# Kernel tuning notes

Measured on AMD Instinct MI355X. Metric: run time of the kernel, lower is better.

The kernel has to match this reference:

```python
import jax, jax.numpy as jnp
import numpy as np

N = 10000    # nodes
D = 128      # d_model
K = 16       # d_state
S = 5        # seq_len (tokens per node)
E = 320000   # edges
R = 200      # num relation types
P = E // (S - 1)  # edges sampled per tokenizer step
EPS = 1e-5


def setup_inputs() -> dict:
    key = jax.random.key(0)
    ks = jax.random.split(key, 16)
    sc = 1.0 / np.sqrt(D)
    return {
        "x": jax.random.normal(ks[0], (N, D), jnp.float32),
        "edge_index": jax.random.randint(ks[1], (2, E), 0, N),
        "edge_type": jax.random.randint(ks[2], (E,), 0, R),
        "perms": jax.random.randint(ks[3], (S - 1, P), 0, E),
        "rel_table": jax.random.normal(ks[4], (R, D), jnp.float32) * 0.1,
        "log_A": jax.random.normal(ks[5], (D, K), jnp.float32) * 0.1,
        "W_B": jax.random.normal(ks[6], (D, K), jnp.float32) * sc,
        "W_C": jax.random.normal(ks[7], (D, K), jnp.float32) * sc,
        "W_delta": jax.random.normal(ks[8], (D, D), jnp.float32) * sc,
        "b_delta": jnp.zeros((D,), jnp.float32),
        "W_g": jax.random.normal(ks[9], (D, D), jnp.float32) * sc,
        "b_g": jnp.zeros((D,), jnp.float32),
        "W_out": jax.random.normal(ks[10], (D, D), jnp.float32) * sc,
        "b_out": jnp.zeros((D,), jnp.float32),
        "ln_g": jnp.ones((D,), jnp.float32),
        "ln_b": jnp.zeros((D,), jnp.float32),
    }


def _tokenize(x, edge_index, edge_type, perms, rel_table):
    # x: [N,D]; perms: [S-1,P] -> tokens [N,S,D]
    src, dst = edge_index[0], edge_index[1]
    step_src = src[perms]                    # [S-1,P]
    step_dst = dst[perms]                    # [S-1,P]
    msg = x[step_src] + rel_table[edge_type[perms]]  # [S-1,P,D]
    seg = jax.vmap(lambda i, m: jax.ops.segment_sum(m, i, num_segments=N))(step_dst, msg)  # [S-1,N,D]
    deg = jax.vmap(lambda i: jax.ops.segment_sum(jnp.ones((P,), x.dtype), i, num_segments=N))(step_dst)  # [S-1,N]
    neigh = seg / jnp.clip(deg, 1.0)[..., None]
    return jnp.concatenate([x[:, None, :], jnp.moveaxis(neigh, 0, 1)], axis=1)  # [N,S,D]


def _selective_scan(tokens, log_A, W_B, W_C, W_delta, b_delta):
    # tokens: [N,S,D] -> [N,S,D]
    deltas = jax.nn.softplus(tokens @ W_delta + b_delta)  # [N,S,D]
    Bs = tokens @ W_B                                     # [N,S,K]
    Cs = tokens @ W_C                                     # [N,S,K]
    A_cont = -jnp.exp(log_A)                              # [D,K]
    A_disc = jnp.exp(deltas[..., None] * A_cont)          # [N,S,D,K]
    Bx = deltas[..., None] * Bs[:, :, None, :] * tokens[..., None]  # [N,S,D,K] = B_disc * x_k

    def step(state, xs):
        a, bx, c = xs                          # [N,D,K],[N,D,K],[N,K]
        state = a * state + bx
        y = jnp.einsum('ndk,nk->nd', state, c)
        return state, y

    init = jnp.zeros((tokens.shape[0], D, K), tokens.dtype)
    _, ys = jax.lax.scan(step, init, (jnp.moveaxis(A_disc, 1, 0),
                                      jnp.moveaxis(Bx, 1, 0),
                                      jnp.moveaxis(Cs, 1, 0)))
    return jnp.moveaxis(ys, 0, 1)  # [N,S,D]


def reference(x, edge_index, edge_type, perms, rel_table, log_A, W_B, W_C,
              W_delta, b_delta, W_g, b_g, W_out, b_out, ln_g, ln_b):
    tokens = _tokenize(x, edge_index, edge_type, perms, rel_table)
    out_f = _selective_scan(tokens, log_A, W_B, W_C, W_delta, b_delta)
    out_b = _selective_scan(tokens[:, ::-1, :], log_A, W_B, W_C, W_delta, b_delta)
    scan_out = (out_f + out_b[:, ::-1, :]).mean(axis=1)  # [N,D]
    gate = jax.nn.silu(x @ W_g + b_g)
    res = x + gate * (scan_out @ W_out + b_out)
    mu = res.mean(axis=-1, keepdims=True)
    var = res.var(axis=-1, keepdims=True)
    return (res - mu) / jnp.sqrt(var + EPS) * ln_g + ln_b
```

## Files before the change

### kernel.cpp

```cpp
#include <hip/hip_runtime.h>
#include <hip/hip_bf16.h>
#include <math.h>

#define N_NODES 10000
#define D_MODEL 128
#define E_EDGES 320000
#define P_EDGES 80000
#define LN_EPS 1e-5f
#define NBUCK 40960
#define CAP 32
#define M_ROWS 50000
#define M_PAD  50048
#define NPAD   320

typedef __attribute__((ext_vector_type(8))) short bf16x8;
typedef __attribute__((ext_vector_type(4))) float f32x4;

__device__ __forceinline__ unsigned short f2bf(float f) {
    __hip_bfloat16 h = __float2bfloat16(f);
    return *reinterpret_cast<unsigned short*>(&h);
}
__device__ __forceinline__ float bf2f(unsigned int u) {
    return __uint_as_float(u << 16);
}

__global__ __launch_bounds__(256) void prep_all(
    const float* __restrict__ Wd, const float* __restrict__ Wb,
    const float* __restrict__ Wc, const float* __restrict__ Wg,
    const float* __restrict__ W_out,
    const float* __restrict__ x, const float* __restrict__ rel,
    const int* __restrict__ edge_index, const int* __restrict__ edge_type,
    unsigned short* __restrict__ Bp, unsigned short* __restrict__ Wop,
    unsigned short* __restrict__ x_bf, unsigned short* __restrict__ rel_bf,
    int* __restrict__ cnt, int4* __restrict__ ed4)
{
    int gid = blockIdx.x * 256 + threadIdx.x;
    if (gid < 40960) {
        int k = gid / NPAD, n = gid - (gid / NPAD) * NPAD;
        float v = 0.f;
        if (n < 128)      v = Wd[k * 128 + n];
        else if (n < 144) v = Wb[k * 16 + (n - 128)];
        else if (n < 160) v = Wc[k * 16 + (n - 144)];
        else if (n < 288) v = Wg[k * 128 + (n - 160)];
        Bp[((size_t)(k >> 3) * NPAD + n) * 8 + (k & 7)] = f2bf(v);
    } else if (gid < 57344) {
        int i = gid - 40960;
        int k = i >> 7, n = i & 127;
        Wop[((size_t)(k >> 3) * 128 + n) * 8 + (k & 7)] = f2bf(W_out[k * 128 + n]);
    } else if (gid < 98304) {
        cnt[gid - 57344] = 0;
    } else if (gid < 123904) {
        int i = gid - 98304;
        rel_bf[i] = f2bf(rel[i]);
    } else if (gid < 1403904) {
        int i = gid - 123904;
        x_bf[i] = f2bf(x[i]);
    } else if (gid < 1723904) {
        int e = gid - 1403904;
        ed4[e] = make_int4(edge_index[e], edge_index[E_EDGES + e], edge_type[e], 0);
    }
}

__global__ __launch_bounds__(256) void csr_build(
    const int4* __restrict__ ed4, const int* __restrict__ perms,
    int* __restrict__ cnt, int2* __restrict__ slots)
{
    int gid = blockIdx.x * blockDim.x + threadIdx.x;
    if (gid >= 4 * P_EDGES) return;
    int s = gid / P_EDGES;
    int e = perms[gid];
    int4 ed = ed4[e];
    int b = ed.y * 4 + s;
    int pos = atomicAdd(&cnt[b], 1);
    if (pos < CAP) slots[(size_t)b * CAP + pos] = make_int2(ed.x, ed.z);
}

__global__ __launch_bounds__(256) void gather_tokens(
    const unsigned short* __restrict__ x_bf,
    const int* __restrict__ cnt, const int2* __restrict__ slots,
    const unsigned short* __restrict__ rel_bf,
    unsigned short* __restrict__ tokens)
{
    int n = blockIdx.x;
    int w = threadIdx.x >> 6, lane = threadIdx.x & 63;
    int b = n * 4 + w;
    int c = cnt[b];
    int cc = c < CAP ? c : CAP;
    const int2* sl = slots + (size_t)b * CAP;
    const unsigned int* xu = (const unsigned int*)x_bf;
    const unsigned int* ru = (const unsigned int*)rel_bf;
    float ax = 0.f, ay = 0.f;
    int j = 0;
    for (; j + 4 <= cc; j += 4) {
        int4 e01 = *(const int4*)(sl + j);
        int4 e23 = *(const int4*)(sl + j + 2);
        unsigned int x0 = xu[(size_t)e01.x * 64 + lane];
        unsigned int r0 = ru[(size_t)e01.y * 64 + lane];
        unsigned int x1 = xu[(size_t)e01.z * 64 + lane];
        unsigned int r1 = ru[(size_t)e01.w * 64 + lane];
        unsigned int x2 = xu[(size_t)e23.x * 64 + lane];
        unsigned int r2 = ru[(size_t)e23.y * 64 + lane];
        unsigned int x3 = xu[(size_t)e23.z * 64 + lane];
        unsigned int r3 = ru[(size_t)e23.w * 64 + lane];
        ax += (bf2f(x0 & 0xffffu) + bf2f(r0 & 0xffffu))
            + (bf2f(x1 & 0xffffu) + bf2f(r1 & 0xffffu))
            + (bf2f(x2 & 0xffffu) + bf2f(r2 & 0xffffu))
            + (bf2f(x3 & 0xffffu) + bf2f(r3 & 0xffffu));
        ay += (bf2f(x0 >> 16) + bf2f(r0 >> 16))
            + (bf2f(x1 >> 16) + bf2f(r1 >> 16))
            + (bf2f(x2 >> 16) + bf2f(r2 >> 16))
            + (bf2f(x3 >> 16) + bf2f(r3 >> 16));
    }
    if (j + 2 <= cc) {
        int4 e01 = *(const int4*)(sl + j);
        unsigned int x0 = xu[(size_t)e01.x * 64 + lane];
        unsigned int r0 = ru[(size_t)e01.y * 64 + lane];
        unsigned int x1 = xu[(size_t)e01.z * 64 + lane];
        unsigned int r1 = ru[(size_t)e01.w * 64 + lane];
        ax += (bf2f(x0 & 0xffffu) + bf2f(r0 & 0xffffu))
            + (bf2f(x1 & 0xffffu) + bf2f(r1 & 0xffffu));
        ay += (bf2f(x0 >> 16) + bf2f(r0 >> 16))
            + (bf2f(x1 >> 16) + bf2f(r1 >> 16));
        j += 2;
    }
    if (j < cc) {
        int2 se = sl[j];
        unsigned int xa = xu[(size_t)se.x * 64 + lane];
        unsigned int ra = ru[(size_t)se.y * 64 + lane];
        ax += bf2f(xa & 0xffffu) + bf2f(ra & 0xffffu);
        ay += bf2f(xa >> 16) + bf2f(ra >> 16);
    }
    float inv = 1.f / fmaxf((float)c, 1.f);
    unsigned int pack = (unsigned int)f2bf(ax * inv)
                      | ((unsigned int)f2bf(ay * inv) << 16);
    ((unsigned int*)tokens)[((size_t)n * 5 + w + 1) * 64 + lane] = pack;
    if (w == 0)
        ((unsigned int*)tokens)[((size_t)n * 5) * 64 + lane] = xu[(size_t)n * 64 + lane];
}

__global__ __launch_bounds__(256) void mfma_gemm(
    const unsigned short* __restrict__ tokens,
    const unsigned short* __restrict__ Bp,
    const float* __restrict__ b_delta, const float* __restrict__ b_g,
    unsigned short* __restrict__ delta,
    unsigned short* __restrict__ bc,
    unsigned short* __restrict__ g)
{
    int m0 = blockIdx.x * 64, n0 = blockIdx.y * 64;
    int wv = threadIdx.x >> 6, lane = threadIdx.x & 63;
    int quad = lane >> 4, l16 = lane & 15;

    f32x4 acc[4] = {{0,0,0,0},{0,0,0,0},{0,0,0,0},{0,0,0,0}};
    const unsigned short* arow = tokens + (size_t)(m0 + wv * 16 + l16) * 128 + quad * 8;
    #pragma unroll
    for (int kc = 0; kc < 128; kc += 32) {
        bf16x8 a = *(const bf16x8*)(arow + kc);
        #pragma unroll
        for (int t = 0; t < 4; ++t) {
            bf16x8 b = *(const bf16x8*)(Bp + ((size_t)(kc / 8 + quad) * NPAD + n0 + 16 * t + l16) * 8);
            acc[t] = __builtin_amdgcn_mfma_f32_16x16x32_bf16(a, b, acc[t], 0, 0, 0);
        }
    }

    int rbase = m0 + wv * 16 + quad * 4;
    #pragma unroll
    for (int t = 0; t < 4; ++t) {
        int c = n0 + 16 * t + l16;
        #pragma unroll
        for (int reg = 0; reg < 4; ++reg) {
            int r = rbase + reg;
            if (r >= M_ROWS) continue;
            float v = acc[t][reg];
            if (c < 128) {
                float z = v + b_delta[c];
                float d = (z > 15.f) ? z : log1pf(__expf(z));
                delta[(size_t)r * 128 + c] = f2bf(d);
            } else if (c < 160) {
                bc[(size_t)r * 32 + (c - 128)] = f2bf(v);
            } else if (c < 288) {
                int rq = r / 5;
                if (r - rq * 5 == 0)
                    g[(size_t)rq * 128 + (c - 160)] = f2bf(v + b_g[c - 160]);
            }
        }
    }
}

__global__ __launch_bounds__(256) void scan_out(
    const unsigned short* __restrict__ tokens,
    const unsigned short* __restrict__ delta,
    const unsigned short* __restrict__ bcbuf,
    const float* __restrict__ log_A,
    const unsigned short* __restrict__ Wop,
    const unsigned short* __restrict__ gbuf,
    const float* __restrict__ x,
    const float* __restrict__ b_out,
    const float* __restrict__ ln_g, const float* __restrict__ ln_b,
    float* __restrict__ out)
{
    int m0 = blockIdx.x * 16;
    int t = threadIdx.x;

    __shared__ float BCs[16][160];
    __shared__ unsigned short soL[16][128];
    __shared__ float res[16 * 132];
    __shared__ float pmu[16][16];
    __shared__ float pv2[16][16];
    __shared__ float muA[16], rstdA[16];

    for (int idx = t; idx < 2560; idx += 256) {
        int n = idx / 160, rem = idx - n * 160;
        int s = rem >> 5, q = rem & 31;
        BCs[n][rem] = bf2f(bcbuf[((size_t)(m0 + n) * 5 + s) * 32 + q]);
    }

    const int d = t & 127;
    float Ac[16];
    {
        const float4* la = (const float4*)(log_A + d * 16);
        #pragma unroll
        for (int q = 0; q < 4; ++q) {
            float4 lv = la[q];
            Ac[q * 4 + 0] = -__expf(lv.x);
            Ac[q * 4 + 1] = -__expf(lv.y);
            Ac[q * 4 + 2] = -__expf(lv.z);
            Ac[q * 4 + 3] = -__expf(lv.w);
        }
    }
    __syncthreads();

    #pragma unroll 1
    for (int i = 0; i < 8; ++i) {
        int n = 2 * i + (t >> 7);
        const unsigned short* tb = tokens + ((size_t)(m0 + n) * 5) * 128 + d;
        const unsigned short* db = delta  + ((size_t)(m0 + n) * 5) * 128 + d;
        float tv[5], dl[5];
        #pragma unroll
        for (int s = 0; s < 5; ++s) {
            tv[s] = bf2f(tb[s * 128]);
            dl[s] = bf2f(db[s * 128]);
        }
        const float* BCn = BCs[n];

        float Af[5][16];
        float total = 0.f;
        {
            float st[16];
            #pragma unroll
            for (int k = 0; k < 16; ++k) st[k] = 0.f;
            #pragma unroll
            for (int s = 0; s < 5; ++s) {
                float dtv = dl[s] * tv[s];
                float y = 0.f;
                #pragma unroll
                for (int k = 0; k < 16; ++k) {
                    float A = __expf(dl[s] * Ac[k]);
                    Af[s][k] = A;
                    st[k] = fmaf(A, st[k], dtv * BCn[s * 32 + k]);
                    y = fmaf(st[k], BCn[s * 32 + 16 + k], y);
                }
                total += y;
            }
        }
        {
            float st[16];
            #pragma unroll
            for (int k = 0; k < 16; ++k) st[k] = 0.f;
            #pragma unroll
            for (int s = 4; s >= 0; --s) {
                float dtv = dl[s] * tv[s];
                float y = 0.f;
                #pragma unroll
                for (int k = 0; k < 16; ++k) {
                    st[k] = fmaf(Af[s][k], st[k], dtv * BCn[s * 32 + k]);
                    y = fmaf(st[k], BCn[s * 32 + 16 + k], y);
                }
                total += y;
            }
        }
        soL[n][d] = f2bf(total * 0.2f);
    }
    __syncthreads();

    int wv = t >> 6, lane = t & 63;
    int quad = lane >> 4, l16 = lane & 15;
    f32x4 acc[2] = {{0,0,0,0},{0,0,0,0}};
    #pragma unroll
    for (int kc = 0; kc < 128; kc += 32) {
        bf16x8 a = *(const bf16x8*)&soL[l16][kc + quad * 8];
        #pragma unroll
        for (int tt = 0; tt < 2; ++tt) {
            int tc = wv * 2 + tt;
            bf16x8 b = *(const bf16x8*)(Wop + ((size_t)(kc / 8 + quad) * 128 + 16 * tc + l16) * 8);
            acc[tt] = __builtin_amdgcn_mfma_f32_16x16x32_bf16(a, b, acc[tt], 0, 0, 0);
        }
    }

    #pragma unroll
    for (int tt = 0; tt < 2; ++tt) {
        int c = wv * 32 + tt * 16 + l16;
        #pragma unroll
        for (int reg = 0; reg < 4; ++reg) {
            int lrow = quad * 4 + reg;
            int r = m0 + lrow;
            float o = acc[tt][reg] + b_out[c];
            float gl = bf2f(gbuf[(size_t)r * 128 + c]);
            float gate = gl / (1.f + __expf(-gl));
            res[lrow * 132 + c] = x[(size_t)r * 128 + c] + gate * o;
        }
    }
    __syncthreads();

    {
        int row = t >> 4, q = t & 15;
        float s = 0.f, s2 = 0.f;
        #pragma unroll
        for (int i = 0; i < 8; ++i) {
            float v = res[row * 132 + q + 16 * i];
            s += v; s2 += v * v;
        }
        pmu[row][q] = s; pv2[row][q] = s2;
    }
    __syncthreads();
    if (t < 16) {
        float s = 0.f, s2 = 0.f;
        #pragma unroll
        for (int i = 0; i < 16; ++i) { s += pmu[t][i]; s2 += pv2[t][i]; }
        float mu = s * (1.f / 128.f);
        float var = s2 * (1.f / 128.f) - mu * mu;
        muA[t] = mu;
        rstdA[t] = rsqrtf(var + LN_EPS);
    }
    __syncthreads();
    #pragma unroll
    for (int i = 0; i < 8; ++i) {
        int idx = i * 256 + t;
        int row = idx >> 7, c = idx & 127;
        out[(size_t)(m0 + row) * 128 + c] =
            (res[row * 132 + c] - muA[row]) * rstdA[row] * ln_g[c] + ln_b[c];
    }
}

extern "C" void kernel_launch(void* const* d_in, const int* in_sizes, int n_in,
                              void* d_out, int out_size, void* d_ws, size_t ws_size,
                              hipStream_t stream) {
    const float* x          = (const float*)d_in[0];
    const int*   edge_index = (const int*)  d_in[1];
    const int*   edge_type  = (const int*)  d_in[2];
    const int*   perms      = (const int*)  d_in[3];
    const float* rel_table  = (const float*)d_in[4];
    const float* log_A      = (const float*)d_in[5];
    const float* W_B        = (const float*)d_in[6];
    const float* W_C        = (const float*)d_in[7];
    const float* W_delta    = (const float*)d_in[8];
    const float* b_delta    = (const float*)d_in[9];
    const float* W_g        = (const float*)d_in[10];
    const float* b_g        = (const float*)d_in[11];
    const float* W_out      = (const float*)d_in[12];
    const float* b_out      = (const float*)d_in[13];
    const float* ln_g       = (const float*)d_in[14];
    const float* ln_b       = (const float*)d_in[15];

    char* ws = (char*)d_ws;
    int*            cnt    = (int*)           (ws + 0);
    unsigned short* Bp     = (unsigned short*)(ws + 163840);
    unsigned short* Wop    = (unsigned short*)(ws + 245760);
    unsigned short* x_bf   = (unsigned short*)(ws + 278528);
    unsigned short* rel_bf = (unsigned short*)(ws + 2838528);
    int4*           ed4    = (int4*)          (ws + 2889728);
    unsigned short* tokens = (unsigned short*)(ws + 8009728);
    unsigned short* g      = (unsigned short*)(ws + 20822016);
    unsigned short* bc     = (unsigned short*)(ws + 23382016);
    int2*           slots  = (int2*)          (ws + 26582016);
    unsigned short* delta  = (unsigned short*)(ws + 26582016);

    prep_all<<<(1723904 + 255) / 256, 256, 0, stream>>>(
        W_delta, W_B, W_C, W_g, W_out, x, rel_table, edge_index, edge_type,
        Bp, Wop, x_bf, rel_bf, cnt, ed4);

    csr_build<<<(4 * P_EDGES + 255) / 256, 256, 0, stream>>>(
        ed4, perms, cnt, slots);

    gather_tokens<<<N_NODES, 256, 0, stream>>>(
        x_bf, cnt, slots, rel_bf, tokens);

    mfma_gemm<<<dim3(M_PAD / 64, NPAD / 64), 256, 0, stream>>>(
        tokens, Bp, b_delta, b_g, delta, bc, g);

    scan_out<<<N_NODES / 16, 256, 0, stream>>>(
        tokens, delta, bc, log_A, Wop, g, x, b_out, ln_g, ln_b, (float*)d_out);
}
```

Baseline: 202.4 us.

## Fuse token gather, projection GEMM and scan into one per-tile kernel

Merges the gather_tokens, mfma_gemm and scan_out kernels into a single kernel that handles 16 nodes per block. Tokens, deltas, B/C and gate values stay in shared memory instead of going through global workspace buffers, which removes two launches and the global round trips of the intermediates. In exchange each block uses about 66KB of LDS, which limits occupancy, and the gather phase now runs on only 625 blocks, so less parallelism is available to hide latency on the irregular loads.

```diff
diff --git a/kernel.cpp b/kernel.cpp
--- a/kernel.cpp
+++ b/kernel.cpp
@@ -9,9 +9,7 @@
 #define LN_EPS 1e-5f
 #define NBUCK 40960
 #define CAP 32
-#define M_ROWS 50000
-#define M_PAD  50048
-#define NPAD   320
+#define NPAD 320
 
 typedef __attribute__((ext_vector_type(8))) short bf16x8;
 typedef __attribute__((ext_vector_type(4))) float f32x4;
@@ -75,144 +73,127 @@
     if (pos < CAP) slots[(size_t)b * CAP + pos] = make_int2(ed.x, ed.z);
 }
 
-__global__ __launch_bounds__(256) void gather_tokens(
+#define TOKS 136
+__global__ __launch_bounds__(256, 2) void fused_main(
     const unsigned short* __restrict__ x_bf,
     const int* __restrict__ cnt, const int2* __restrict__ slots,
     const unsigned short* __restrict__ rel_bf,
-    unsigned short* __restrict__ tokens)
-{
-    int n = blockIdx.x;
-    int w = threadIdx.x >> 6, lane = threadIdx.x & 63;
-    int b = n * 4 + w;
-    int c = cnt[b];
-    int cc = c < CAP ? c : CAP;
-    const int2* sl = slots + (size_t)b * CAP;
-    const unsigned int* xu = (const unsigned int*)x_bf;
-    const unsigned int* ru = (const unsigned int*)rel_bf;
-    float ax = 0.f, ay = 0.f;
-    int j = 0;
-    for (; j + 4 <= cc; j += 4) {
-        int4 e01 = *(const int4*)(sl + j);
-        int4 e23 = *(const int4*)(sl + j + 2);
-        unsigned int x0 = xu[(size_t)e01.x * 64 + lane];
-        unsigned int r0 = ru[(size_t)e01.y * 64 + lane];
-        unsigned int x1 = xu[(size_t)e01.z * 64 + lane];
-        unsigned int r1 = ru[(size_t)e01.w * 64 + lane];
-        unsigned int x2 = xu[(size_t)e23.x * 64 + lane];
-        unsigned int r2 = ru[(size_t)e23.y * 64 + lane];
-        unsigned int x3 = xu[(size_t)e23.z * 64 + lane];
-        unsigned int r3 = ru[(size_t)e23.w * 64 + lane];
-        ax += (bf2f(x0 & 0xffffu) + bf2f(r0 & 0xffffu))
-            + (bf2f(x1 & 0xffffu) + bf2f(r1 & 0xffffu))
-            + (bf2f(x2 & 0xffffu) + bf2f(r2 & 0xffffu))
-            + (bf2f(x3 & 0xffffu) + bf2f(r3 & 0xffffu));
-        ay += (bf2f(x0 >> 16) + bf2f(r0 >> 16))
-            + (bf2f(x1 >> 16) + bf2f(r1 >> 16))
-            + (bf2f(x2 >> 16) + bf2f(r2 >> 16))
-            + (bf2f(x3 >> 16) + bf2f(r3 >> 16));
-    }
-    if (j + 2 <= cc) {
-        int4 e01 = *(const int4*)(sl + j);
-        unsigned int x0 = xu[(size_t)e01.x * 64 + lane];
-        unsigned int r0 = ru[(size_t)e01.y * 64 + lane];
-        unsigned int x1 = xu[(size_t)e01.z * 64 + lane];
-        unsigned int r1 = ru[(size_t)e01.w * 64 + lane];
-        ax += (bf2f(x0 & 0xffffu) + bf2f(r0 & 0xffffu))
-            + (bf2f(x1 & 0xffffu) + bf2f(r1 & 0xffffu));
-        ay += (bf2f(x0 >> 16) + bf2f(r0 >> 16))
-            + (bf2f(x1 >> 16) + bf2f(r1 >> 16));
-        j += 2;
-    }
-    if (j < cc) {
-        int2 se = sl[j];
-        unsigned int xa = xu[(size_t)se.x * 64 + lane];
-        unsigned int ra = ru[(size_t)se.y * 64 + lane];
-        ax += bf2f(xa & 0xffffu) + bf2f(ra & 0xffffu);
-        ay += bf2f(xa >> 16) + bf2f(ra >> 16);
-    }
-    float inv = 1.f / fmaxf((float)c, 1.f);
-    unsigned int pack = (unsigned int)f2bf(ax * inv)
-                      | ((unsigned int)f2bf(ay * inv) << 16);
-    ((unsigned int*)tokens)[((size_t)n * 5 + w + 1) * 64 + lane] = pack;
-    if (w == 0)
-        ((unsigned int*)tokens)[((size_t)n * 5) * 64 + lane] = xu[(size_t)n * 64 + lane];
-}
-
-__global__ __launch_bounds__(256) void mfma_gemm(
-    const unsigned short* __restrict__ tokens,
     const unsigned short* __restrict__ Bp,
+    const unsigned short* __restrict__ Wop,
+    const float* __restrict__ log_A,
     const float* __restrict__ b_delta, const float* __restrict__ b_g,
-    unsigned short* __restrict__ delta,
-    unsigned short* __restrict__ bc,
-    unsigned short* __restrict__ g)
-{
-    int m0 = blockIdx.x * 64, n0 = blockIdx.y * 64;
-    int wv = threadIdx.x >> 6, lane = threadIdx.x & 63;
-    int quad = lane >> 4, l16 = lane & 15;
-
-    f32x4 acc[4] = {{0,0,0,0},{0,0,0,0},{0,0,0,0},{0,0,0,0}};
-    const unsigned short* arow = tokens + (size_t)(m0 + wv * 16 + l16) * 128 + quad * 8;
-    #pragma unroll
-    for (int kc = 0; kc < 128; kc += 32) {
-        bf16x8 a = *(const bf16x8*)(arow + kc);
-        #pragma unroll
-        for (int t = 0; t < 4; ++t) {
-            bf16x8 b = *(const bf16x8*)(Bp + ((size_t)(kc / 8 + quad) * NPAD + n0 + 16 * t + l16) * 8);
-            acc[t] = __builtin_amdgcn_mfma_f32_16x16x32_bf16(a, b, acc[t], 0, 0, 0);
-        }
-    }
-
-    int rbase = m0 + wv * 16 + quad * 4;
-    #pragma unroll
-    for (int t = 0; t < 4; ++t) {
-        int c = n0 + 16 * t + l16;
-        #pragma unroll
-        for (int reg = 0; reg < 4; ++reg) {
-            int r = rbase + reg;
-            if (r >= M_ROWS) continue;
-            float v = acc[t][reg];
-            if (c < 128) {
-                float z = v + b_delta[c];
-                float d = (z > 15.f) ? z : log1pf(__expf(z));
-                delta[(size_t)r * 128 + c] = f2bf(d);
-            } else if (c < 160) {
-                bc[(size_t)r * 32 + (c - 128)] = f2bf(v);
-            } else if (c < 288) {
-                int rq = r / 5;
-                if (r - rq * 5 == 0)
-                    g[(size_t)rq * 128 + (c - 160)] = f2bf(v + b_g[c - 160]);
-            }
-        }
-    }
-}
-
-__global__ __launch_bounds__(256) void scan_out(
-    const unsigned short* __restrict__ tokens,
-    const unsigned short* __restrict__ delta,
-    const unsigned short* __restrict__ bcbuf,
-    const float* __restrict__ log_A,
-    const unsigned short* __restrict__ Wop,
-    const unsigned short* __restrict__ gbuf,
     const float* __restrict__ x,
     const float* __restrict__ b_out,
     const float* __restrict__ ln_g, const float* __restrict__ ln_b,
     float* __restrict__ out)
 {
-    int m0 = blockIdx.x * 16;
-    int t = threadIdx.x;
-
-    __shared__ float BCs[16][160];
-    __shared__ unsigned short soL[16][128];
-    __shared__ float res[16 * 132];
-    __shared__ float pmu[16][16];
-    __shared__ float pv2[16][16];
-    __shared__ float muA[16], rstdA[16];
-
-    for (int idx = t; idx < 2560; idx += 256) {
-        int n = idx / 160, rem = idx - n * 160;
-        int s = rem >> 5, q = rem & 31;
-        BCs[n][rem] = bf2f(bcbuf[((size_t)(m0 + n) * 5 + s) * 32 + q]);
-    }
+    const int n0 = blockIdx.x * 16;
+    const int t = threadIdx.x;
+    const int wv = t >> 6, lane = t & 63;
+    const int quad = lane >> 4, l16 = lane & 15;
+
+    __shared__ __align__(16) char smem[66304];
+    unsigned short* tokL = (unsigned short*)smem;
+    unsigned short* dltL = (unsigned short*)(smem + 21760);
+    float*          bcL  = (float*)(smem + 43520);
+    float*          gL   = (float*)(smem + 53760);
+    unsigned short* soL  = (unsigned short*)(smem + 61952);
+    float* res   = (float*)smem;
+    float* pmu   = (float*)(smem + 8448);
+    float* pv2   = (float*)(smem + 9472);
+    float* muA   = (float*)(smem + 10496);
+    float* rstdA = (float*)(smem + 10560);
+
+    const unsigned int* xu = (const unsigned int*)x_bf;
+    const unsigned int* ru = (const unsigned int*)rel_bf;
+
+    for (int idx = t; idx < 1024; idx += 256) {
+        int i = idx >> 6, ln2 = idx & 63;
+        ((unsigned int*)&tokL[(i * 5) * TOKS])[ln2] = xu[(size_t)(n0 + i) * 64 + ln2];
+    }
+    for (int q = 0; q < 16; ++q) {
+        int bl = wv * 16 + q;
+        int i = bl >> 2, s = bl & 3;
+        int B = (n0 + i) * 4 + s;
+        int c = cnt[B];
+        int cc = c < CAP ? c : CAP;
+        const int2* sl = slots + (size_t)B * CAP;
+        float ax = 0.f, ay = 0.f;
+        int j = 0;
+        for (; j + 4 <= cc; j += 4) {
+            int4 e01 = *(const int4*)(sl + j);
+            int4 e23 = *(const int4*)(sl + j + 2);
+            unsigned int x0 = xu[(size_t)e01.x * 64 + lane];
+            unsigned int r0 = ru[(size_t)e01.y * 64 + lane];
+            unsigned int x1 = xu[(size_t)e01.z * 64 + lane];
+            unsigned int r1 = ru[(size_t)e01.w * 64 + lane];
+            unsigned int x2 = xu[(size_t)e23.x * 64 + lane];
+            unsigned int r2 = ru[(size_t)e23.y * 64 + lane];
+            unsigned int x3 = xu[(size_t)e23.z * 64 + lane];
+            unsigned int r3 = ru[(size_t)e23.w * 64 + lane];
+            ax += (bf2f(x0 & 0xffffu) + bf2f(r0 & 0xffffu))
+                + (bf2f(x1 & 0xffffu) + bf2f(r1 & 0xffffu))
+                + (bf2f(x2 & 0xffffu) + bf2f(r2 & 0xffffu))
+                + (bf2f(x3 & 0xffffu) + bf2f(r3 & 0xffffu));
+            ay += (bf2f(x0 >> 16) + bf2f(r0 >> 16))
+                + (bf2f(x1 >> 16) + bf2f(r1 >> 16))
+                + (bf2f(x2 >> 16) + bf2f(r2 >> 16))
+                + (bf2f(x3 >> 16) + bf2f(r3 >> 16));
+        }
+        if (j + 2 <= cc) {
+            int4 e01 = *(const int4*)(sl + j);
+            unsigned int x0 = xu[(size_t)e01.x * 64 + lane];
+            unsigned int r0 = ru[(size_t)e01.y * 64 + lane];
+            unsigned int x1 = xu[(size_t)e01.z * 64 + lane];
+            unsigned int r1 = ru[(size_t)e01.w * 64 + lane];
+            ax += (bf2f(x0 & 0xffffu) + bf2f(r0 & 0xffffu))
+                + (bf2f(x1 & 0xffffu) + bf2f(r1 & 0xffffu));
+            ay += (bf2f(x0 >> 16) + bf2f(r0 >> 16))
+                + (bf2f(x1 >> 16) + bf2f(r1 >> 16));
+            j += 2;
+        }
+        if (j < cc) {
+            int2 se = sl[j];
+            unsigned int xa = xu[(size_t)se.x * 64 + lane];
+            unsigned int ra = ru[(size_t)se.y * 64 + lane];
+            ax += bf2f(xa & 0xffffu) + bf2f(ra & 0xffffu);
+            ay += bf2f(xa >> 16) + bf2f(ra >> 16);
+        }
+        float inv = 1.f / fmaxf((float)c, 1.f);
+        unsigned int pack = (unsigned int)f2bf(ax * inv)
+                          | ((unsigned int)f2bf(ay * inv) << 16);
+        *(unsigned int*)&tokL[(i * 5 + s + 1) * TOKS + 2 * lane] = pack;
+    }
+    __syncthreads();
+
+    for (int tt = wv; tt < 90; tt += 4) {
+        int mt = tt / 18, nt = tt - mt * 18;
+        f32x4 acc = {0, 0, 0, 0};
+        #pragma unroll
+        for (int kc = 0; kc < 4; ++kc) {
+            bf16x8 a = *(const bf16x8*)&tokL[(mt * 16 + l16) * TOKS + kc * 32 + quad * 8];
+            bf16x8 b = *(const bf16x8*)(Bp + ((size_t)(kc * 4 + quad) * NPAD + nt * 16 + l16) * 8);
+            acc = __builtin_amdgcn_mfma_f32_16x16x32_bf16(a, b, acc, 0, 0, 0);
+        }
+        int c = nt * 16 + l16;
+        #pragma unroll
+        for (int reg = 0; reg < 4; ++reg) {
+            int lr = mt * 16 + quad * 4 + reg;
+            float v = acc[reg];
+            if (c < 128) {
+                float z = v + b_delta[c];
+                float d = (z > 15.f) ? z : log1pf(__expf(z));
+                dltL[lr * TOKS + c] = f2bf(d);
+            } else if (c < 160) {
+                bcL[lr * 32 + (c - 128)] = v;
+            } else {
+                int rq = lr / 5;
+                if (lr - rq * 5 == 0)
+                    gL[rq * 128 + (c - 160)] = v + b_g[c - 160];
+            }
+        }
+    }
+    __syncthreads();
 
     const int d = t & 127;
     float Ac[16];
@@ -227,20 +208,16 @@
             Ac[q * 4 + 3] = -__expf(lv.w);
         }
     }
-    __syncthreads();
-
     #pragma unroll 1
     for (int i = 0; i < 8; ++i) {
-        int n = 2 * i + (t >> 7);
-        const unsigned short* tb = tokens + ((size_t)(m0 + n) * 5) * 128 + d;
-        const unsigned short* db = delta  + ((size_t)(m0 + n) * 5) * 128 + d;
+        int nl = 2 * i + (t >> 7);
         float tv[5], dl[5];
         #pragma unroll
         for (int s = 0; s < 5; ++s) {
-            tv[s] = bf2f(tb[s * 128]);
-            dl[s] = bf2f(db[s * 128]);
-        }
-        const float* BCn = BCs[n];
+            tv[s] = bf2f(tokL[(nl * 5 + s) * TOKS + d]);
+            dl[s] = bf2f(dltL[(nl * 5 + s) * TOKS + d]);
+        }
+        const float* BCn = &bcL[nl * 5 * 32];
 
         float Af[5][16];
         float total = 0.f;
@@ -278,35 +255,42 @@
                 total += y;
             }
         }
-        soL[n][d] = f2bf(total * 0.2f);
-    }
-    __syncthreads();
-
-    int wv = t >> 6, lane = t & 63;
-    int quad = lane >> 4, l16 = lane & 15;
+        soL[nl * TOKS + d] = f2bf(total * 0.2f);
+    }
+    __syncthreads();
+
     f32x4 acc[2] = {{0,0,0,0},{0,0,0,0}};
     #pragma unroll
-    for (int kc = 0; kc < 128; kc += 32) {
-        bf16x8 a = *(const bf16x8*)&soL[l16][kc + quad * 8];
+    for (int kc = 0; kc < 4; ++kc) {
+        bf16x8 a = *(const bf16x8*)&soL[l16 * TOKS + kc * 32 + quad * 8];
         #pragma unroll
         for (int tt = 0; tt < 2; ++tt) {
             int tc = wv * 2 + tt;
-            bf16x8 b = *(const bf16x8*)(Wop + ((size_t)(kc / 8 + quad) * 128 + 16 * tc + l16) * 8);
+            bf16x8 b = *(const bf16x8*)(Wop + ((size_t)(kc * 4 + quad) * 128 + 16 * tc + l16) * 8);
             acc[tt] = __builtin_amdgcn_mfma_f32_16x16x32_bf16(a, b, acc[tt], 0, 0, 0);
         }
     }
-
+    float rv[2][4];
     #pragma unroll
     for (int tt = 0; tt < 2; ++tt) {
         int c = wv * 32 + tt * 16 + l16;
         #pragma unroll
         for (int reg = 0; reg < 4; ++reg) {
             int lrow = quad * 4 + reg;
-            int r = m0 + lrow;
             float o = acc[tt][reg] + b_out[c];
-            float gl = bf2f(gbuf[(size_t)r * 128 + c]);
+            float gl = gL[lrow * 128 + c];
             float gate = gl / (1.f + __expf(-gl));
-            res[lrow * 132 + c] = x[(size_t)r * 128 + c] + gate * o;
+            rv[tt][reg] = x[(size_t)(n0 + lrow) * 128 + c] + gate * o;
+        }
+    }
+    __syncthreads();
+    #pragma unroll
+    for (int tt = 0; tt < 2; ++tt) {
+        int c = wv * 32 + tt * 16 + l16;
+        #pragma unroll
+        for (int reg = 0; reg < 4; ++reg) {
+            int lrow = quad * 4 + reg;
+            res[lrow * 132 + c] = rv[tt][reg];
         }
     }
     __syncthreads();
@@ -319,13 +303,13 @@
             float v = res[row * 132 + q + 16 * i];
             s += v; s2 += v * v;
         }
-        pmu[row][q] = s; pv2[row][q] = s2;
+        pmu[row * 16 + q] = s; pv2[row * 16 + q] = s2;
     }
     __syncthreads();
     if (t < 16) {
         float s = 0.f, s2 = 0.f;
         #pragma unroll
-        for (int i = 0; i < 16; ++i) { s += pmu[t][i]; s2 += pv2[t][i]; }
+        for (int i = 0; i < 16; ++i) { s += pmu[t * 16 + i]; s2 += pv2[t * 16 + i]; }
         float mu = s * (1.f / 128.f);
         float var = s2 * (1.f / 128.f) - mu * mu;
         muA[t] = mu;
@@ -336,7 +320,7 @@
     for (int i = 0; i < 8; ++i) {
         int idx = i * 256 + t;
         int row = idx >> 7, c = idx & 127;
-        out[(size_t)(m0 + row) * 128 + c] =
+        out[(size_t)(n0 + row) * 128 + c] =
             (res[row * 132 + c] - muA[row]) * rstdA[row] * ln_g[c] + ln_b[c];
     }
 }
@@ -368,11 +352,7 @@
     unsigned short* x_bf   = (unsigned short*)(ws + 278528);
     unsigned short* rel_bf = (unsigned short*)(ws + 2838528);
     int4*           ed4    = (int4*)          (ws + 2889728);
-    unsigned short* tokens = (unsigned short*)(ws + 8009728);
-    unsigned short* g      = (unsigned short*)(ws + 20822016);
-    unsigned short* bc     = (unsigned short*)(ws + 23382016);
-    int2*           slots  = (int2*)          (ws + 26582016);
-    unsigned short* delta  = (unsigned short*)(ws + 26582016);
+    int2*           slots  = (int2*)          (ws + 8009728);
 
     prep_all<<<(1723904 + 255) / 256, 256, 0, stream>>>(
         W_delta, W_B, W_C, W_g, W_out, x, rel_table, edge_index, edge_type,
@@ -381,12 +361,7 @@
     csr_build<<<(4 * P_EDGES + 255) / 256, 256, 0, stream>>>(
         ed4, perms, cnt, slots);
 
-    gather_tokens<<<N_NODES, 256, 0, stream>>>(
-        x_bf, cnt, slots, rel_bf, tokens);
-
-    mfma_gemm<<<dim3(M_PAD / 64, NPAD / 64), 256, 0, stream>>>(
-        tokens, Bp, b_delta, b_g, delta, bc, g);
-
-    scan_out<<<N_NODES / 16, 256, 0, stream>>>(
-        tokens, delta, bc, log_A, Wop, g, x, b_out, ln_g, ln_b, (float*)d_out);
-}
+    fused_main<<<N_NODES / 16, 256, 0, stream>>>(
+        x_bf, cnt, slots, rel_bf, Bp, Wop, log_A, b_delta, b_g,
+        x, b_out, ln_g, ln_b, (float*)d_out);
+}
```

New measurement: 256.7 us. 1.27x slower.

## Widen scan_out to 512 threads, alias shared memory, write x token in prep

Applied to the files above, without the earlier changes.

scan_out now runs with 512 threads per block. Each thread processes 4 node-rows instead of 8, and each wave computes a single 16-column MFMA tile for the output projection. Shared memory is packed into one aliased buffer, with the residual tile overlapping the BC staging area. A padded soL stride reduces LDS bank conflicts. The copy of x into token slot 0 moves from gather_tokens into prep_all. The changes aim to raise parallelism and occupancy in the scan epilogue and remove redundant work from gather, but they add a redundant zero store and rely on an extra barrier to make the aliasing safe.

```diff
diff --git a/kernel.cpp b/kernel.cpp
--- a/kernel.cpp
+++ b/kernel.cpp
@@ -32,7 +32,8 @@
     const int* __restrict__ edge_index, const int* __restrict__ edge_type,
     unsigned short* __restrict__ Bp, unsigned short* __restrict__ Wop,
     unsigned short* __restrict__ x_bf, unsigned short* __restrict__ rel_bf,
-    int* __restrict__ cnt, int4* __restrict__ ed4)
+    int* __restrict__ cnt, int4* __restrict__ ed4,
+    unsigned short* __restrict__ tokens)
 {
     int gid = blockIdx.x * 256 + threadIdx.x;
     if (gid < 40960) {
@@ -54,7 +55,9 @@
         rel_bf[i] = f2bf(rel[i]);
     } else if (gid < 1403904) {
         int i = gid - 123904;
-        x_bf[i] = f2bf(x[i]);
+        unsigned short v = f2bf(x[i]);
+        x_bf[i] = v;
+        tokens[(size_t)(i >> 7) * 640 + (i & 127)] = v;
     } else if (gid < 1723904) {
         int e = gid - 1403904;
         ed4[e] = make_int4(edge_index[e], edge_index[E_EDGES + e], edge_type[e], 0);
@@ -134,8 +137,6 @@
     unsigned int pack = (unsigned int)f2bf(ax * inv)
                       | ((unsigned int)f2bf(ay * inv) << 16);
     ((unsigned int*)tokens)[((size_t)n * 5 + w + 1) * 64 + lane] = pack;
-    if (w == 0)
-        ((unsigned int*)tokens)[((size_t)n * 5) * 64 + lane] = xu[(size_t)n * 64 + lane];
 }
 
 __global__ __launch_bounds__(256) void mfma_gemm(
@@ -186,7 +187,8 @@
     }
 }
 
-__global__ __launch_bounds__(256) void scan_out(
+#define SOS 136
+__global__ __launch_bounds__(512) void scan_out(
     const unsigned short* __restrict__ tokens,
     const unsigned short* __restrict__ delta,
     const unsigned short* __restrict__ bcbuf,
@@ -198,20 +200,25 @@
     const float* __restrict__ ln_g, const float* __restrict__ ln_b,
     float* __restrict__ out)
 {
-    int m0 = blockIdx.x * 16;
-    int t = threadIdx.x;
-
-    __shared__ float BCs[16][160];
-    __shared__ unsigned short soL[16][128];
-    __shared__ float res[16 * 132];
-    __shared__ float pmu[16][16];
-    __shared__ float pv2[16][16];
-    __shared__ float muA[16], rstdA[16];
-
-    for (int idx = t; idx < 2560; idx += 256) {
+    const int m0 = blockIdx.x * 16;
+    const int t = threadIdx.x;
+    const int wv = t >> 6, lane = t & 63;
+    const int quad = lane >> 4, l16 = lane & 15;
+
+    __shared__ __align__(16) char smem[19136];
+    float*          BCs = (float*)smem;
+    unsigned short* soL = (unsigned short*)(smem + 10240);
+    float* pmu   = (float*)(smem + 14592);
+    float* pv2   = (float*)(smem + 16640);
+    float* muA   = (float*)(smem + 18688);
+    float* rstdA = (float*)(smem + 18752);
+    float* res   = (float*)smem;
+
+    for (int idx = t; idx < 2560; idx += 512) {
         int n = idx / 160, rem = idx - n * 160;
         int s = rem >> 5, q = rem & 31;
-        BCs[n][rem] = bf2f(bcbuf[((size_t)(m0 + n) * 5 + s) * 32 + q]);
+        BCs[n * 160 + rem - (s << 5) + s * 32 + q - q] = 0.f;
+        BCs[n * 160 + rem] = bf2f(bcbuf[((size_t)(m0 + n) * 5 + s) * 32 + q]);
     }
 
     const int d = t & 127;
@@ -230,17 +237,17 @@
     __syncthreads();
 
     #pragma unroll 1
-    for (int i = 0; i < 8; ++i) {
-        int n = 2 * i + (t >> 7);
-        const unsigned short* tb = tokens + ((size_t)(m0 + n) * 5) * 128 + d;
-        const unsigned short* db = delta  + ((size_t)(m0 + n) * 5) * 128 + d;
+    for (int i = 0; i < 4; ++i) {
+        int nl = 4 * i + (t >> 7);
+        const unsigned short* tb = tokens + ((size_t)(m0 + nl) * 5) * 128 + d;
+        const unsigned short* db = delta  + ((size_t)(m0 + nl) * 5) * 128 + d;
         float tv[5], dl[5];
         #pragma unroll
         for (int s = 0; s < 5; ++s) {
             tv[s] = bf2f(tb[s * 128]);
             dl[s] = bf2f(db[s * 128]);
         }
-        const float* BCn = BCs[n];
+        const float* BCn = &BCs[nl * 160];
 
         float Af[5][16];
         float total = 0.f;
@@ -278,54 +285,52 @@
                 total += y;
             }
         }
-        soL[n][d] = f2bf(total * 0.2f);
-    }
-    __syncthreads();
-
-    int wv = t >> 6, lane = t & 63;
-    int quad = lane >> 4, l16 = lane & 15;
-    f32x4 acc[2] = {{0,0,0,0},{0,0,0,0}};
+        soL[nl * SOS + d] = f2bf(total * 0.2f);
+    }
+    __syncthreads();
+
+    f32x4 acc = {0, 0, 0, 0};
     #pragma unroll
-    for (int kc = 0; kc < 128; kc += 32) {
-        bf16x8 a = *(const bf16x8*)&soL[l16][kc + quad * 8];
-        #pragma unroll
-        for (int tt = 0; tt < 2; ++tt) {
-            int tc = wv * 2 + tt;
-            bf16x8 b = *(const bf16x8*)(Wop + ((size_t)(kc / 8 + quad) * 128 + 16 * tc + l16) * 8);
-            acc[tt] = __builtin_amdgcn_mfma_f32_16x16x32_bf16(a, b, acc[tt], 0, 0, 0);
-        }
-    }
-
-    #pragma unroll
-    for (int tt = 0; tt < 2; ++tt) {
-        int c = wv * 32 + tt * 16 + l16;
+    for (int kc = 0; kc < 4; ++kc) {
+        bf16x8 a = *(const bf16x8*)&soL[l16 * SOS + kc * 32 + quad * 8];
+        bf16x8 b = *(const bf16x8*)(Wop + ((size_t)(kc * 4 + quad) * 128 + 16 * wv + l16) * 8);
+        acc = __builtin_amdgcn_mfma_f32_16x16x32_bf16(a, b, acc, 0, 0, 0);
+    }
+    {
+        int c = wv * 16 + l16;
+        float rv[4];
         #pragma unroll
         for (int reg = 0; reg < 4; ++reg) {
             int lrow = quad * 4 + reg;
-            int r = m0 + lrow;
-            float o = acc[tt][reg] + b_out[c];
-            float gl = bf2f(gbuf[(size_t)r * 128 + c]);
+            float o = acc[reg] + b_out[c];
+            float gl = bf2f(gbuf[(size_t)(m0 + lrow) * 128 + c]);
             float gate = gl / (1.f + __expf(-gl));
-            res[lrow * 132 + c] = x[(size_t)r * 128 + c] + gate * o;
+            rv[reg] = x[(size_t)(m0 + lrow) * 128 + c] + gate * o;
+        }
+        __syncthreads();
+        #pragma unroll
+        for (int reg = 0; reg < 4; ++reg) {
+            int lrow = quad * 4 + reg;
+            res[lrow * 132 + c] = rv[reg];
         }
     }
     __syncthreads();
 
     {
-        int row = t >> 4, q = t & 15;
+        int row = t >> 5, q = t & 31;
         float s = 0.f, s2 = 0.f;
         #pragma unroll
-        for (int i = 0; i < 8; ++i) {
-            float v = res[row * 132 + q + 16 * i];
+        for (int i = 0; i < 4; ++i) {
+            float v = res[row * 132 + q + 32 * i];
             s += v; s2 += v * v;
         }
-        pmu[row][q] = s; pv2[row][q] = s2;
+        pmu[row * 32 + q] = s; pv2[row * 32 + q] = s2;
     }
     __syncthreads();
     if (t < 16) {
         float s = 0.f, s2 = 0.f;
         #pragma unroll
-        for (int i = 0; i < 16; ++i) { s += pmu[t][i]; s2 += pv2[t][i]; }
+        for (int i = 0; i < 32; ++i) { s += pmu[t * 32 + i]; s2 += pv2[t * 32 + i]; }
         float mu = s * (1.f / 128.f);
         float var = s2 * (1.f / 128.f) - mu * mu;
         muA[t] = mu;
@@ -333,8 +338,8 @@
     }
     __syncthreads();
     #pragma unroll
-    for (int i = 0; i < 8; ++i) {
-        int idx = i * 256 + t;
+    for (int i = 0; i < 4; ++i) {
+        int idx = i * 512 + t;
         int row = idx >> 7, c = idx & 127;
         out[(size_t)(m0 + row) * 128 + c] =
             (res[row * 132 + c] - muA[row]) * rstdA[row] * ln_g[c] + ln_b[c];
@@ -376,7 +381,7 @@
 
     prep_all<<<(1723904 + 255) / 256, 256, 0, stream>>>(
         W_delta, W_B, W_C, W_g, W_out, x, rel_table, edge_index, edge_type,
-        Bp, Wop, x_bf, rel_bf, cnt, ed4);
+        Bp, Wop, x_bf, rel_bf, cnt, ed4, tokens);
 
     csr_build<<<(4 * P_EDGES + 255) / 256, 256, 0, stream>>>(
         ed4, perms, cnt, slots);
@@ -387,6 +392,6 @@
     mfma_gemm<<<dim3(M_PAD / 64, NPAD / 64), 256, 0, stream>>>(
         tokens, Bp, b_delta, b_g, delta, bc, g);
 
-    scan_out<<<N_NODES / 16, 256, 0, stream>>>(
+    scan_out<<<N_NODES / 16, 512, 0, stream>>>(
         tokens, delta, bc, log_A, Wop, g, x, b_out, ln_g, ln_b, (float*)d_out);
 }
```

Result: slower. 211.1 us (+4.3%).

## Fuse forward and backward scans into one pass, write token 0 in prep

Applied to the files above, without the earlier changes.

The backward selective scan is folded into the forward loop algebraically. A running suffix vector V of C values, decayed by the same A factors, gives the backward contribution as dtv*dot(V,B). This drops the stored Af[5][16] array and the second pass of 80 FMAs per node-channel, which cuts register pressure. Separately, prep_all now writes the bf16 copy of x directly into token slot 0, so gather_tokens no longer does that extra read and write. The rewritten reduction changes floating-point summation order slightly.

```diff
diff --git a/kernel.cpp b/kernel.cpp
--- a/kernel.cpp
+++ b/kernel.cpp
@@ -32,7 +32,8 @@
     const int* __restrict__ edge_index, const int* __restrict__ edge_type,
     unsigned short* __restrict__ Bp, unsigned short* __restrict__ Wop,
     unsigned short* __restrict__ x_bf, unsigned short* __restrict__ rel_bf,
-    int* __restrict__ cnt, int4* __restrict__ ed4)
+    int* __restrict__ cnt, int4* __restrict__ ed4,
+    unsigned short* __restrict__ tokens)
 {
     int gid = blockIdx.x * 256 + threadIdx.x;
     if (gid < 40960) {
@@ -54,7 +55,9 @@
         rel_bf[i] = f2bf(rel[i]);
     } else if (gid < 1403904) {
         int i = gid - 123904;
-        x_bf[i] = f2bf(x[i]);
+        unsigned short v = f2bf(x[i]);
+        x_bf[i] = v;
+        tokens[(size_t)(i >> 7) * 640 + (i & 127)] = v;
     } else if (gid < 1723904) {
         int e = gid - 1403904;
         ed4[e] = make_int4(edge_index[e], edge_index[E_EDGES + e], edge_type[e], 0);
@@ -134,8 +137,6 @@
     unsigned int pack = (unsigned int)f2bf(ax * inv)
                       | ((unsigned int)f2bf(ay * inv) << 16);
     ((unsigned int*)tokens)[((size_t)n * 5 + w + 1) * 64 + lane] = pack;
-    if (w == 0)
-        ((unsigned int*)tokens)[((size_t)n * 5) * 64 + lane] = xu[(size_t)n * 64 + lane];
 }
 
 __global__ __launch_bounds__(256) void mfma_gemm(
@@ -186,6 +187,7 @@
     }
 }
 
+#define SOS 136
 __global__ __launch_bounds__(256) void scan_out(
     const unsigned short* __restrict__ tokens,
     const unsigned short* __restrict__ delta,
@@ -198,14 +200,15 @@
     const float* __restrict__ ln_g, const float* __restrict__ ln_b,
     float* __restrict__ out)
 {
-    int m0 = blockIdx.x * 16;
-    int t = threadIdx.x;
-
-    __shared__ float BCs[16][160];
-    __shared__ unsigned short soL[16][128];
-    __shared__ float res[16 * 132];
-    __shared__ float pmu[16][16];
-    __shared__ float pv2[16][16];
+    const int m0 = blockIdx.x * 16;
+    const int t = threadIdx.x;
+    const int wv = t >> 6, lane = t & 63;
+    const int quad = lane >> 4, l16 = lane & 15;
+
+    __shared__ __align__(16) float BCs[16][160];
+    __shared__ __align__(16) unsigned short soL[16][SOS];
+    __shared__ float res[16][132];
+    __shared__ float pmu[16][16], pv2[16][16];
     __shared__ float muA[16], rstdA[16];
 
     for (int idx = t; idx < 2560; idx += 256) {
@@ -231,82 +234,62 @@
 
     #pragma unroll 1
     for (int i = 0; i < 8; ++i) {
-        int n = 2 * i + (t >> 7);
-        const unsigned short* tb = tokens + ((size_t)(m0 + n) * 5) * 128 + d;
-        const unsigned short* db = delta  + ((size_t)(m0 + n) * 5) * 128 + d;
+        int nl = 2 * i + (t >> 7);
+        const unsigned short* tb = tokens + ((size_t)(m0 + nl) * 5) * 128 + d;
+        const unsigned short* db = delta  + ((size_t)(m0 + nl) * 5) * 128 + d;
         float tv[5], dl[5];
         #pragma unroll
         for (int s = 0; s < 5; ++s) {
             tv[s] = bf2f(tb[s * 128]);
             dl[s] = bf2f(db[s * 128]);
         }
-        const float* BCn = BCs[n];
-
-        float Af[5][16];
+        const float* BCn = &BCs[nl][0];
+
+        float st[16], V[16];
+        #pragma unroll
+        for (int k = 0; k < 16; ++k) { st[k] = 0.f; V[k] = BCn[16 + k]; }
         float total = 0.f;
-        {
-            float st[16];
+        #pragma unroll
+        for (int s = 0; s < 5; ++s) {
+            float dtv = dl[s] * tv[s];
+            float yf = 0.f, ub = 0.f;
             #pragma unroll
-            for (int k = 0; k < 16; ++k) st[k] = 0.f;
-            #pragma unroll
-            for (int s = 0; s < 5; ++s) {
-                float dtv = dl[s] * tv[s];
-                float y = 0.f;
-                #pragma unroll
-                for (int k = 0; k < 16; ++k) {
-                    float A = __expf(dl[s] * Ac[k]);
-                    Af[s][k] = A;
-                    st[k] = fmaf(A, st[k], dtv * BCn[s * 32 + k]);
-                    y = fmaf(st[k], BCn[s * 32 + 16 + k], y);
-                }
-                total += y;
+            for (int k = 0; k < 16; ++k) {
+                float B = BCn[s * 32 + k];
+                float C = BCn[s * 32 + 16 + k];
+                float A = __expf(dl[s] * Ac[k]);
+                st[k] = fmaf(A, st[k], dtv * B);
+                yf = fmaf(st[k], C, yf);
+                ub = fmaf(V[k], B, ub);
+                if (s < 4) V[k] = fmaf(A, V[k], BCn[(s + 1) * 32 + 16 + k]);
             }
-        }
-        {
-            float st[16];
-            #pragma unroll
-            for (int k = 0; k < 16; ++k) st[k] = 0.f;
-            #pragma unroll
-            for (int s = 4; s >= 0; --s) {
-                float dtv = dl[s] * tv[s];
-                float y = 0.f;
-                #pragma unroll
-                for (int k = 0; k < 16; ++k) {
-                    st[k] = fmaf(Af[s][k], st[k], dtv * BCn[s * 32 + k]);
-                    y = fmaf(st[k], BCn[s * 32 + 16 + k], y);
-                }
-                total += y;
-            }
-        }
-        soL[n][d] = f2bf(total * 0.2f);
-    }
-    __syncthreads();
-
-    int wv = t >> 6, lane = t & 63;
-    int quad = lane >> 4, l16 = lane & 15;
+            total += yf + dtv * ub;
+        }
+        soL[nl][d] = f2bf(total * 0.2f);
+    }
+    __syncthreads();
+
     f32x4 acc[2] = {{0,0,0,0},{0,0,0,0}};
     #pragma unroll
-    for (int kc = 0; kc < 128; kc += 32) {
-        bf16x8 a = *(const bf16x8*)&soL[l16][kc + quad * 8];
+    for (int kc = 0; kc < 4; ++kc) {
+        bf16x8 a = *(const bf16x8*)&soL[l16][kc * 32 + quad * 8];
         #pragma unroll
         for (int tt = 0; tt < 2; ++tt) {
             int tc = wv * 2 + tt;
-            bf16x8 b = *(const bf16x8*)(Wop + ((size_t)(kc / 8 + quad) * 128 + 16 * tc + l16) * 8);
+            bf16x8 b = *(const bf16x8*)(Wop + ((size_t)(kc * 4 + quad) * 128 + 16 * tc + l16) * 8);
             acc[tt] = __builtin_amdgcn_mfma_f32_16x16x32_bf16(a, b, acc[tt], 0, 0, 0);
         }
     }
-
     #pragma unroll
     for (int tt = 0; tt < 2; ++tt) {
         int c = wv * 32 + tt * 16 + l16;
         #pragma unroll
         for (int reg = 0; reg < 4; ++reg) {
             int lrow = quad * 4 + reg;
-            int r = m0 + lrow;
             float o = acc[tt][reg] + b_out[c];
-            float gl = bf2f(gbuf[(size_t)r * 128 + c]);
+            float gl = bf2f(gbuf[(size_t)(m0 + lrow) * 128 + c]);
             float gate = gl / (1.f + __expf(-gl));
-            res[lrow * 132 + c] = x[(size_t)r * 128 + c] + gate * o;
+            res[lrow][c] = x[(size_t)(m0 + lrow) * 128 + c] + gate * o;
         }
     }
     __syncthreads();
@@ -316,7 +299,7 @@
         float s = 0.f, s2 = 0.f;
         #pragma unroll
         for (int i = 0; i < 8; ++i) {
-            float v = res[row * 132 + q + 16 * i];
+            float v = res[row][q + 16 * i];
             s += v; s2 += v * v;
         }
         pmu[row][q] = s; pv2[row][q] = s2;
@@ -337,7 +320,7 @@
         int idx = i * 256 + t;
         int row = idx >> 7, c = idx & 127;
         out[(size_t)(m0 + row) * 128 + c] =
-            (res[row * 132 + c] - muA[row]) * rstdA[row] * ln_g[c] + ln_b[c];
+            (res[row][c] - muA[row]) * rstdA[row] * ln_g[c] + ln_b[c];
     }
 }
 
@@ -376,7 +359,7 @@
 
     prep_all<<<(1723904 + 255) / 256, 256, 0, stream>>>(
         W_delta, W_B, W_C, W_g, W_out, x, rel_table, edge_index, edge_type,
-        Bp, Wop, x_bf, rel_bf, cnt, ed4);
+        Bp, Wop, x_bf, rel_bf, cnt, ed4, tokens);
 
     csr_build<<<(4 * P_EDGES + 255) / 256, 256, 0, stream>>>(
         ed4, perms, cnt, slots);
```

Measured after the change: 219.4 us. +8.4%, slower.
